# Kernel optimization log

Measured on AMD Instinct MI355X. Metric: run time of the kernel, lower is better.

Reference implementation:

```python
import jax, jax.numpy as jnp
import numpy as np

B, N, C = 8, 1024, 768
H = 12
D = C // H            # 64
HID = int(C * 4.0)    # 3072
SCALE = D ** -0.5
EPS_LN = 1e-5
EPS_BN = 1e-5


def _layernorm(x, g, b):
    mu = jnp.mean(x, axis=-1, keepdims=True)
    var = jnp.mean(jnp.square(x - mu), axis=-1, keepdims=True)
    return (x - mu) * jax.lax.rsqrt(var + EPS_LN) * g + b


def setup_inputs() -> dict:
    key = jax.random.key(0)
    ks = jax.random.split(key, 12)
    s = lambda fan: 1.0 / np.sqrt(fan)
    inp = {
        "inputs": jax.random.normal(ks[0], (B, N, C), jnp.float32),
        "ln1_g": jnp.ones((C,), jnp.float32),
        "ln1_b": jnp.zeros((C,), jnp.float32),
        # nn.Linear(dim, 3*dim, bias=False)
        "qkv_w": jax.random.uniform(ks[1], (3 * C, C), jnp.float32, -s(C), s(C)),
        # nn.Conv2d(H, H, 1, 1) head-mixing matrix
        "conv_w": jax.random.uniform(ks[2], (H, H), jnp.float32, -s(H), s(H)),
        "conv_b": jax.random.uniform(ks[3], (H,), jnp.float32, -s(H), s(H)),
        # BatchNorm2d(H) in eval mode: affine params + running stats
        "bn_g": jnp.ones((H,), jnp.float32),
        "bn_b": jnp.zeros((H,), jnp.float32),
        "bn_rm": jnp.zeros((H,), jnp.float32),
        "bn_rv": jnp.ones((H,), jnp.float32),
        "proj_w": jax.random.uniform(ks[4], (C, C), jnp.float32, -s(C), s(C)),
        "proj_b": jax.random.uniform(ks[5], (C,), jnp.float32, -s(C), s(C)),
        "ln2_g": jnp.ones((C,), jnp.float32),
        "ln2_b": jnp.zeros((C,), jnp.float32),
        "fc1_w": jax.random.uniform(ks[6], (HID, C), jnp.float32, -s(C), s(C)),
        "fc1_b": jax.random.uniform(ks[7], (HID,), jnp.float32, -s(C), s(C)),
        "fc2_w": jax.random.uniform(ks[8], (C, HID), jnp.float32, -s(HID), s(HID)),
        "fc2_b": jax.random.uniform(ks[9], (C,), jnp.float32, -s(HID), s(HID)),
    }
    return inp


def reference(inputs, ln1_g, ln1_b, qkv_w, conv_w, conv_b, bn_g, bn_b, bn_rm, bn_rv,
              proj_w, proj_b, ln2_g, ln2_b, fc1_w, fc1_b, fc2_w, fc2_b):
    # adjust_ratio = 1.0, dropouts are identity (inference), BN uses running stats (eval)
    x_ln = _layernorm(inputs, ln1_g, ln1_b)
    qkv = (x_ln @ qkv_w.T).reshape(B, N, 3, H, D).transpose(2, 0, 3, 1, 4)
    q, k, v = qkv[0], qkv[1], qkv[2]
    attn = jax.nn.softmax(jnp.einsum('bhnd,bhmd->bhnm', q, k) * SCALE, axis=-1)
    # 1x1 conv across heads then BatchNorm2d (eval) * reatten_scale(=1.0)
    attn = jnp.einsum('oh,bhnm->bonm', conv_w, attn) + conv_b[None, :, None, None]
    bn_scale = bn_g * jax.lax.rsqrt(bn_rv + EPS_BN)
    attn = (attn - bn_rm[None, :, None, None]) * bn_scale[None, :, None, None] \
        + bn_b[None, :, None, None]
    attn_next = attn
    out = jnp.einsum('bhnm,bhmd->bhnd', attn, v).transpose(0, 2, 1, 3).reshape(B, N, C)
    out = out @ proj_w.T + proj_b
    x = inputs + out
    h = _layernorm(x, ln2_g, ln2_b)
    h = jax.nn.gelu(h @ fc1_w.T + fc1_b, approximate=False)
    x = x + (h @ fc2_w.T + fc2_b)
    return (x, attn_next)
```

## Files before the change

### kernel.cpp

```cpp
#include <hip/hip_runtime.h>
#include <cmath>

#define B_   8
#define N_   1024
#define C_   768
#define H_   12
#define D_   64
#define HID_ 3072
#define M_   8192

using frag  = __attribute__((ext_vector_type(8))) short;
using f32x4 = __attribute__((ext_vector_type(4))) float;
using s4v   = __attribute__((ext_vector_type(4))) short;

__device__ __forceinline__ short f2bf(float x) {
    union { float f; unsigned u; } v; v.f = x;
    unsigned r = (v.u + 0x7FFFu + ((v.u >> 16) & 1u)) >> 16;
    return (short)r;
}
__device__ __forceinline__ float b2f(short s) {
    union { float f; unsigned u; } v; v.u = ((unsigned)(unsigned short)s) << 16;
    return v.f;
}
__device__ __forceinline__ float bfr(float x) { return b2f(f2bf(x)); }
__device__ __forceinline__ float gelu_exact(float x) {
    return 0.5f * x * (1.0f + erff(x * 0.70710678118654752f));
}
__device__ __forceinline__ void gload16(const void* g, void* l) {
    __builtin_amdgcn_global_load_lds(
        (const __attribute__((address_space(1))) void*)g,
        (__attribute__((address_space(3))) void*)l, 16, 0, 0);
}

__global__ __launch_bounds__(256)
void cvt_bf16(const float* __restrict__ src, short* __restrict__ dst, int n)
{
    int i = (blockIdx.x * 256 + threadIdx.x) * 4;
    if (i < n) {
        float4 u = *(const float4*)(src + i);
        s4v s; s[0] = f2bf(u.x); s[1] = f2bf(u.y); s[2] = f2bf(u.z); s[3] = f2bf(u.w);
        *(s4v*)(dst + i) = s;
    }
}

__global__ __launch_bounds__(256)
void ln_bf16(const float* __restrict__ x, const float* __restrict__ g,
             const float* __restrict__ b, short* __restrict__ y)
{
    __shared__ float red[256];
    const long row = blockIdx.x;
    const float* xr = x + row * C_;
    short* yr = y + row * C_;
    const int t = threadIdx.x;
    float v0 = xr[t], v1 = xr[t + 256], v2 = xr[t + 512];
    red[t] = v0 + v1 + v2;
    __syncthreads();
    for (int o = 128; o > 0; o >>= 1) { if (t < o) red[t] += red[t + o]; __syncthreads(); }
    const float mu = red[0] * (1.0f / 768.0f);
    __syncthreads();
    const float d0 = v0 - mu, d1 = v1 - mu, d2 = v2 - mu;
    red[t] = d0 * d0 + d1 * d1 + d2 * d2;
    __syncthreads();
    for (int o = 128; o > 0; o >>= 1) { if (t < o) red[t] += red[t + o]; __syncthreads(); }
    const float rstd = rsqrtf(red[0] * (1.0f / 768.0f) + 1e-5f);
    yr[t]       = f2bf(d0 * rstd * g[t]       + b[t]);
    yr[t + 256] = f2bf(d1 * rstd * g[t + 256] + b[t + 256]);
    yr[t + 512] = f2bf(d2 * rstd * g[t + 512] + b[t + 512]);
}

template<int BM, int BN, int WGM, int WGN, bool AF32, bool OUTF32, bool ACT_GELU, bool STATS>
__global__ __launch_bounds__(256)
void gemm_mfma(const void* __restrict__ Ap, int lda, long sAb, long sAh,
               const short* __restrict__ Bp, int ldb, long sBb, long sBh,
               const float* __restrict__ bias,
               const float* __restrict__ res, int ldres,
               void* __restrict__ Cp, int ldc, long sCb, long sCh,
               float2* __restrict__ st,
               int K, float alpha)
{
    constexpr int FM = BM / (WGM * 16), FN = BN / (WGN * 16);
    __shared__ short As[BM * 64];
    __shared__ short Bs[BN * 64];
    const int tid = threadIdx.x;
    const int wid = tid >> 6, lane = tid & 63;
    const int z = blockIdx.z, zb = z / H_, zh = z - zb * H_;
    const long m0 = (long)blockIdx.y * BM;
    const int  n0 = blockIdx.x * BN;
    const short* Bb = Bp + zb * sBb + zh * sBh + (long)n0 * ldb;
    const short* Abh = nullptr; const float* Afh = nullptr;
    if constexpr (AF32) Afh = (const float*)Ap + zb * sAb + zh * sAh + m0 * lda;
    else                Abh = (const short*)Ap + zb * sAb + zh * sAh + m0 * lda;
    f32x4 acc[FM][FN] = {};
    const int wr = wid / WGN, wc = wid - wr * WGN;
    const int srow = lane >> 3;
    const int schunk = (lane & 7) ^ srow;

    for (int k0 = 0; k0 < K; k0 += 64) {
        if constexpr (!AF32) {
            for (int g = wid; g < BM / 8; g += 4)
                gload16(Abh + (long)(g * 8 + srow) * lda + k0 + schunk * 8, &As[g * 512]);
        } else {
            const int r = tid >> 1, h2 = tid & 1;
            const float* sp = Afh + (long)r * lda + k0 + h2 * 32;
            #pragma unroll
            for (int j = 0; j < 4; ++j) {
                float4 u0 = *(const float4*)(sp + j * 8);
                float4 u1 = *(const float4*)(sp + j * 8 + 4);
                frag w;
                w[0] = f2bf(u0.x); w[1] = f2bf(u0.y); w[2] = f2bf(u0.z); w[3] = f2bf(u0.w);
                w[4] = f2bf(u1.x); w[5] = f2bf(u1.y); w[6] = f2bf(u1.z); w[7] = f2bf(u1.w);
                *(frag*)&As[r * 64 + (((h2 * 4 + j)) ^ (r & 7)) * 8] = w;
            }
        }
        for (int g = wid; g < BN / 8; g += 4)
            gload16(Bb + (long)(g * 8 + srow) * ldb + k0 + schunk * 8, &Bs[g * 512]);
        __syncthreads();
        #pragma unroll
        for (int kk = 0; kk < 2; ++kk) {
            frag a[FM], b[FN];
            #pragma unroll
            for (int fm = 0; fm < FM; ++fm) {
                const int r = wr * FM * 16 + fm * 16 + (lane & 15);
                const int ph = (kk * 4 + (lane >> 4)) ^ (r & 7);
                a[fm] = *(const frag*)&As[r * 64 + ph * 8];
            }
            #pragma unroll
            for (int fn = 0; fn < FN; ++fn) {
                const int r = wc * FN * 16 + fn * 16 + (lane & 15);
                const int ph = (kk * 4 + (lane >> 4)) ^ (r & 7);
                b[fn] = *(const frag*)&Bs[r * 64 + ph * 8];
            }
            #pragma unroll
            for (int fm = 0; fm < FM; ++fm)
                #pragma unroll
                for (int fn = 0; fn < FN; ++fn)
                    acc[fm][fn] = __builtin_amdgcn_mfma_f32_16x16x32_bf16(a[fm], b[fn], acc[fm][fn], 0, 0, 0);
        }
        __syncthreads();
    }

    float* Cf = (float*)Cp; short* Cs = (short*)Cp;
    const long cbase = zb * sCb + zh * sCh;
    #pragma unroll
    for (int fm = 0; fm < FM; ++fm) {
        #pragma unroll
        for (int fn = 0; fn < FN; ++fn) {
            const long rg = m0 + wr * FM * 16 + fm * 16 + ((lane >> 4) * 4);
            const int  cg = n0 + wc * FN * 16 + fn * 16 + (lane & 15);
            const float bv = bias ? bias[cg] : 0.0f;
            #pragma unroll
            for (int q = 0; q < 4; ++q) {
                const long row = rg + q;
                float v = acc[fm][fn][q] * alpha + bv;
                if (res) v += res[row * (long)ldres + cg];
                if constexpr (ACT_GELU) v = gelu_exact(v);
                if constexpr (OUTF32) Cf[cbase + row * ldc + cg] = v;
                else                  Cs[cbase + row * ldc + cg] = f2bf(v);
            }
        }
    }

    if constexpr (STATS) {
        float* sred = (float*)As;
        float tmax[FM][4];
        #pragma unroll
        for (int fm = 0; fm < FM; ++fm)
            #pragma unroll
            for (int q = 0; q < 4; ++q) {
                float v = bfr(acc[fm][0][q] * alpha);
                #pragma unroll
                for (int fn = 1; fn < FN; ++fn) v = fmaxf(v, bfr(acc[fm][fn][q] * alpha));
                v = fmaxf(v, __shfl_xor(v, 1));
                v = fmaxf(v, __shfl_xor(v, 2));
                v = fmaxf(v, __shfl_xor(v, 4));
                v = fmaxf(v, __shfl_xor(v, 8));
                const int r = wr * FM * 16 + fm * 16 + (lane >> 4) * 4 + q;
                if ((lane & 15) == 0) sred[wc * BM + r] = v;
            }
        __syncthreads();
        #pragma unroll
        for (int fm = 0; fm < FM; ++fm)
            #pragma unroll
            for (int q = 0; q < 4; ++q) {
                const int r = wr * FM * 16 + fm * 16 + (lane >> 4) * 4 + q;
                tmax[fm][q] = fmaxf(sred[r], sred[BM + r]);
            }
        __syncthreads();
        #pragma unroll
        for (int fm = 0; fm < FM; ++fm)
            #pragma unroll
            for (int q = 0; q < 4; ++q) {
                float e = 0.0f;
                #pragma unroll
                for (int fn = 0; fn < FN; ++fn)
                    e += __expf(bfr(acc[fm][fn][q] * alpha) - tmax[fm][q]);
                e += __shfl_xor(e, 1);
                e += __shfl_xor(e, 2);
                e += __shfl_xor(e, 4);
                e += __shfl_xor(e, 8);
                const int r = wr * FM * 16 + fm * 16 + (lane >> 4) * 4 + q;
                if ((lane & 15) == 0) sred[wc * BM + r] = e;
            }
        __syncthreads();
        if (wc == 0) {
            #pragma unroll
            for (int fm = 0; fm < FM; ++fm)
                #pragma unroll
                for (int q = 0; q < 4; ++q) {
                    const int r = wr * FM * 16 + fm * 16 + (lane >> 4) * 4 + q;
                    if ((lane & 15) == 0) {
                        float2 o; o.x = tmax[fm][q]; o.y = sred[r] + sred[BM + r];
                        st[((long)z * N_ + m0 + r) * 8 + blockIdx.x] = o;
                    }
                }
        }
    }
}

__global__ __launch_bounds__(256)
void smb2(const short* __restrict__ S, const float2* __restrict__ st,
          float* __restrict__ attn,
          const float* __restrict__ cw, const float* __restrict__ cb,
          const float* __restrict__ bg, const float* __restrict__ bb,
          const float* __restrict__ brm, const float* __restrict__ brv)
{
    __shared__ float coef[H_][H_], baseA[H_], scA[H_], smx[H_], sinv[H_];
    const int t = threadIdx.x;
    const int bn = blockIdx.x;
    const int b = bn >> 10, n = bn & 1023;
    if (t < H_) {
        const float s = bg[t] * rsqrtf(brv[t] + 1e-5f);
        scA[t] = s;
        baseA[t] = (cb[t] - brm[t]) * s + bb[t];
    }
    __syncthreads();
    if (t < H_ * H_) coef[t / H_][t % H_] = cw[t] * scA[t / H_];
    if (t < H_) {
        const float2* sp = st + ((long)(b * H_ + t) * N_ + n) * 8;
        float2 sv[8];
        #pragma unroll
        for (int i = 0; i < 8; ++i) sv[i] = sp[i];
        float gm = sv[0].x;
        #pragma unroll
        for (int i = 1; i < 8; ++i) gm = fmaxf(gm, sv[i].x);
        float gs = 0.0f;
        #pragma unroll
        for (int i = 0; i < 8; ++i) gs += sv[i].y * __expf(sv[i].x - gm);
        smx[t] = gm;
        sinv[t] = 1.0f / gs;
    }
    __syncthreads();

    const long pstr = (long)N_ * N_;
    const short* sb = S    + (long)b * H_ * pstr + (long)n * N_ + t * 4;
    float*       ab = attn + (long)b * H_ * pstr + (long)n * N_ + t * 4;
    float4 p[H_];
    #pragma unroll
    for (int h = 0; h < H_; ++h) {
        const s4v sv = *(const s4v*)(sb + (long)h * pstr);
        const float gm = smx[h], gi = sinv[h];
        float4 e;
        e.x = __expf(b2f(sv[0]) - gm) * gi;
        e.y = __expf(b2f(sv[1]) - gm) * gi;
        e.z = __expf(b2f(sv[2]) - gm) * gi;
        e.w = __expf(b2f(sv[3]) - gm) * gi;
        p[h] = e;
    }
    #pragma unroll
    for (int o = 0; o < H_; ++o) {
        const float bse = baseA[o];
        float4 a; a.x = bse; a.y = bse; a.z = bse; a.w = bse;
        #pragma unroll
        for (int h = 0; h < H_; ++h) {
            const float w = coef[o][h];
            a.x += w * p[h].x; a.y += w * p[h].y;
            a.z += w * p[h].z; a.w += w * p[h].w;
        }
        *(float4*)(ab + (long)o * pstr) = a;
    }
}

__global__ __launch_bounds__(256)
void vtrans(const short* __restrict__ qkv, short* __restrict__ vT)
{
    __shared__ short tile[64][72];
    const int bh = blockIdx.x;
    const int n0 = blockIdx.y * 64;
    const int b = bh / H_, h = bh - b * H_;
    const short* src = qkv + (long)b * N_ * (3 * C_) + 2 * C_ + h * D_;
    const int t = threadIdx.x;
    {
        const int r = t >> 2, c = (t & 3) * 16;
        const short* sp = src + (long)(n0 + r) * (3 * C_) + c;
        #pragma unroll
        for (int j = 0; j < 16; j++) tile[r][c + j] = sp[j];
    }
    __syncthreads();
    {
        const int d = t >> 2, c = (t & 3) * 16;
        short* dp = vT + (long)bh * (D_ * N_) + (long)d * N_ + n0 + c;
        #pragma unroll
        for (int j = 0; j < 16; j++) dp[j] = tile[c + j][d];
    }
}

extern "C" void kernel_launch(void* const* d_in, const int* in_sizes, int n_in,
                              void* d_out, int out_size, void* d_ws, size_t ws_size,
                              hipStream_t stream)
{
    const float* inp    = (const float*)d_in[0];
    const float* ln1_g  = (const float*)d_in[1];
    const float* ln1_b  = (const float*)d_in[2];
    const float* qkv_w  = (const float*)d_in[3];
    const float* conv_w = (const float*)d_in[4];
    const float* conv_b = (const float*)d_in[5];
    const float* bn_g   = (const float*)d_in[6];
    const float* bn_b   = (const float*)d_in[7];
    const float* bn_rm  = (const float*)d_in[8];
    const float* bn_rv  = (const float*)d_in[9];
    const float* proj_w = (const float*)d_in[10];
    const float* proj_b = (const float*)d_in[11];
    const float* ln2_g  = (const float*)d_in[12];
    const float* ln2_b  = (const float*)d_in[13];
    const float* fc1_w  = (const float*)d_in[14];
    const float* fc1_b  = (const float*)d_in[15];
    const float* fc2_w  = (const float*)d_in[16];
    const float* fc2_b  = (const float*)d_in[17];

    float* outx = (float*)d_out;
    float* attn = outx + (long)M_ * C_;

    char* w = (char*)d_ws;
    short* wqkv  = (short*)w;  w += (long)3 * C_ * C_ * 2;
    short* wproj = (short*)w;  w += (long)C_ * C_ * 2;
    short* wfc1  = (short*)w;  w += (long)HID_ * C_ * 2;
    short* wfc2  = (short*)w;  w += (long)C_ * HID_ * 2;
    short* xln   = (short*)w;  w += (long)M_ * C_ * 2;
    short* qkvb  = (short*)w;
    short* hbuf  = qkvb;       w += (long)M_ * HID_ * 2;
    short* vT    = (short*)w;  w += (long)B_ * H_ * D_ * N_ * 2;
    short* Obf   = (short*)w;  w += (long)M_ * C_ * 2;
    float* xres  = (float*)w;  w += (long)M_ * C_ * 4;
    float2* st   = (float2*)w; w += (long)B_ * H_ * N_ * 8 * 8;
    short* Sbf   = (short*)w;  w += (long)B_ * H_ * N_ * N_ * 2;

    cvt_bf16<<<(3 * C_ * C_) / 1024, 256, 0, stream>>>(qkv_w, wqkv, 3 * C_ * C_);
    cvt_bf16<<<(C_ * C_) / 1024,     256, 0, stream>>>(proj_w, wproj, C_ * C_);
    cvt_bf16<<<(HID_ * C_) / 1024,   256, 0, stream>>>(fc1_w, wfc1, HID_ * C_);
    cvt_bf16<<<(C_ * HID_) / 1024,   256, 0, stream>>>(fc2_w, wfc2, C_ * HID_);

    ln_bf16<<<M_, 256, 0, stream>>>(inp, ln1_g, ln1_b, xln);

    gemm_mfma<128, 128, 2, 2, false, false, false, false><<<dim3(18, 64, 1), 256, 0, stream>>>(
        xln, C_, 0, 0, wqkv, C_, 0, 0, nullptr, nullptr, 0,
        qkvb, 3 * C_, 0, 0, nullptr, C_, 1.0f);

    vtrans<<<dim3(B_ * H_, 16), 256, 0, stream>>>(qkvb, vT);

    gemm_mfma<128, 128, 2, 2, false, false, false, true><<<dim3(8, 8, 96), 256, 0, stream>>>(
        qkvb,      3 * C_, (long)N_ * 3 * C_, D_,
        qkvb + C_, 3 * C_, (long)N_ * 3 * C_, D_,
        nullptr, nullptr, 0,
        Sbf, N_, (long)H_ * N_ * N_, (long)N_ * N_, st, D_, 0.125f);

    smb2<<<M_, 256, 0, stream>>>(Sbf, st, attn, conv_w, conv_b, bn_g, bn_b, bn_rm, bn_rv);

    gemm_mfma<128, 64, 4, 1, true, false, false, false><<<dim3(1, 8, 96), 256, 0, stream>>>(
        attn, N_, (long)H_ * N_ * N_, (long)N_ * N_,
        vT, N_, (long)H_ * D_ * N_, (long)D_ * N_,
        nullptr, nullptr, 0,
        Obf, C_, (long)N_ * C_, D_, nullptr, N_, 1.0f);

    gemm_mfma<128, 128, 2, 2, false, true, false, false><<<dim3(6, 64, 1), 256, 0, stream>>>(
        Obf, C_, 0, 0, wproj, C_, 0, 0, proj_b, inp, C_,
        xres, C_, 0, 0, nullptr, C_, 1.0f);

    ln_bf16<<<M_, 256, 0, stream>>>(xres, ln2_g, ln2_b, xln);

    gemm_mfma<128, 128, 2, 2, false, false, true, false><<<dim3(24, 64, 1), 256, 0, stream>>>(
        xln, C_, 0, 0, wfc1, C_, 0, 0, fc1_b, nullptr, 0,
        hbuf, HID_, 0, 0, nullptr, C_, 1.0f);

    gemm_mfma<128, 128, 2, 2, false, true, false, false><<<dim3(6, 64, 1), 256, 0, stream>>>(
        hbuf, HID_, 0, 0, wfc2, HID_, 0, 0, fc2_b, xres, C_,
        outx, C_, 0, 0, nullptr, HID_, 1.0f);
}
```

Before: 649.3 us.

## Write bf16 attention copy in smb2, swizzle GEMM blocks across XCDs, merge weight casts

The softmax/conv/BN kernel now also writes a bf16 copy of the attention map into the score buffer. The attn@V GEMM can then load its A operand with direct global-to-LDS loads instead of reading fp32 attention and converting it in registers. GEMM workgroup IDs are remapped so consecutive tiles land on the same XCD for better L2 reuse, and the four weight-cast launches are merged into one. The cost is an extra 200MB-class bf16 write of the attention map, traded against halving the attn@V A-operand read bandwidth and its conversion work.

```diff
diff --git a/kernel.cpp b/kernel.cpp
--- a/kernel.cpp
+++ b/kernel.cpp
@@ -32,15 +32,36 @@
         (__attribute__((address_space(3))) void*)l, 16, 0, 0);
 }
 
-__global__ __launch_bounds__(256)
-void cvt_bf16(const float* __restrict__ src, short* __restrict__ dst, int n)
-{
-    int i = (blockIdx.x * 256 + threadIdx.x) * 4;
-    if (i < n) {
-        float4 u = *(const float4*)(src + i);
-        s4v s; s[0] = f2bf(u.x); s[1] = f2bf(u.y); s[2] = f2bf(u.z); s[3] = f2bf(u.w);
-        *(s4v*)(dst + i) = s;
-    }
+__device__ __forceinline__ int2 swz_xy() {
+    const int gx = gridDim.x;
+    const int nwg = gx * gridDim.y;
+    const int orig = blockIdx.y * gx + blockIdx.x;
+    const int q = nwg >> 3, r = nwg & 7;
+    const int xcd = orig & 7;
+    const int base = (xcd < r) ? xcd * (q + 1) : r * (q + 1) + (xcd - r) * q;
+    const int wgid = base + (orig >> 3);
+    int2 v; v.x = wgid % gx; v.y = wgid / gx;
+    return v;
+}
+
+#define NW0 (3 * C_ * C_)
+#define NW1 (C_ * C_)
+#define NW2 (HID_ * C_)
+#define NW3 (C_ * HID_)
+__global__ __launch_bounds__(256)
+void cvt_weights(const float* __restrict__ s0, const float* __restrict__ s1,
+                 const float* __restrict__ s2, const float* __restrict__ s3,
+                 short* __restrict__ dst)
+{
+    long i = ((long)blockIdx.x * 256 + threadIdx.x) * 4;
+    const float* s; long off;
+    if      (i < NW0)             { s = s0; off = i; }
+    else if (i < NW0 + NW1)       { s = s1; off = i - NW0; }
+    else if (i < NW0 + NW1 + NW2) { s = s2; off = i - NW0 - NW1; }
+    else                          { s = s3; off = i - NW0 - NW1 - NW2; }
+    float4 u = *(const float4*)(s + off);
+    s4v o; o[0] = f2bf(u.x); o[1] = f2bf(u.y); o[2] = f2bf(u.z); o[3] = f2bf(u.w);
+    *(s4v*)(dst + i) = o;
 }
 
 __global__ __launch_bounds__(256)
@@ -68,9 +89,9 @@
     yr[t + 512] = f2bf(d2 * rstd * g[t + 512] + b[t + 512]);
 }
 
-template<int BM, int BN, int WGM, int WGN, bool AF32, bool OUTF32, bool ACT_GELU, bool STATS>
-__global__ __launch_bounds__(256)
-void gemm_mfma(const void* __restrict__ Ap, int lda, long sAb, long sAh,
+template<int BM, int BN, int WGM, int WGN, bool OUTF32, bool ACT_GELU, bool STATS>
+__global__ __launch_bounds__(256)
+void gemm_mfma(const short* __restrict__ Ap, int lda, long sAb, long sAh,
                const short* __restrict__ Bp, int ldb, long sBb, long sBh,
                const float* __restrict__ bias,
                const float* __restrict__ res, int ldres,
@@ -84,34 +105,20 @@
     const int tid = threadIdx.x;
     const int wid = tid >> 6, lane = tid & 63;
     const int z = blockIdx.z, zb = z / H_, zh = z - zb * H_;
-    const long m0 = (long)blockIdx.y * BM;
-    const int  n0 = blockIdx.x * BN;
+    const int2 bxy = swz_xy();
+    const int bx = bxy.x, by = bxy.y;
+    const long m0 = (long)by * BM;
+    const int  n0 = bx * BN;
+    const short* Ab = Ap + zb * sAb + zh * sAh + m0 * lda;
     const short* Bb = Bp + zb * sBb + zh * sBh + (long)n0 * ldb;
-    const short* Abh = nullptr; const float* Afh = nullptr;
-    if constexpr (AF32) Afh = (const float*)Ap + zb * sAb + zh * sAh + m0 * lda;
-    else                Abh = (const short*)Ap + zb * sAb + zh * sAh + m0 * lda;
     f32x4 acc[FM][FN] = {};
     const int wr = wid / WGN, wc = wid - wr * WGN;
     const int srow = lane >> 3;
     const int schunk = (lane & 7) ^ srow;
 
     for (int k0 = 0; k0 < K; k0 += 64) {
-        if constexpr (!AF32) {
-            for (int g = wid; g < BM / 8; g += 4)
-                gload16(Abh + (long)(g * 8 + srow) * lda + k0 + schunk * 8, &As[g * 512]);
-        } else {
-            const int r = tid >> 1, h2 = tid & 1;
-            const float* sp = Afh + (long)r * lda + k0 + h2 * 32;
-            #pragma unroll
-            for (int j = 0; j < 4; ++j) {
-                float4 u0 = *(const float4*)(sp + j * 8);
-                float4 u1 = *(const float4*)(sp + j * 8 + 4);
-                frag w;
-                w[0] = f2bf(u0.x); w[1] = f2bf(u0.y); w[2] = f2bf(u0.z); w[3] = f2bf(u0.w);
-                w[4] = f2bf(u1.x); w[5] = f2bf(u1.y); w[6] = f2bf(u1.z); w[7] = f2bf(u1.w);
-                *(frag*)&As[r * 64 + (((h2 * 4 + j)) ^ (r & 7)) * 8] = w;
-            }
-        }
+        for (int g = wid; g < BM / 8; g += 4)
+            gload16(Ab + (long)(g * 8 + srow) * lda + k0 + schunk * 8, &As[g * 512]);
         for (int g = wid; g < BN / 8; g += 4)
             gload16(Bb + (long)(g * 8 + srow) * ldb + k0 + schunk * 8, &Bs[g * 512]);
         __syncthreads();
@@ -210,7 +217,7 @@
                     const int r = wr * FM * 16 + fm * 16 + (lane >> 4) * 4 + q;
                     if ((lane & 15) == 0) {
                         float2 o; o.x = tmax[fm][q]; o.y = sred[r] + sred[BM + r];
-                        st[((long)z * N_ + m0 + r) * 8 + blockIdx.x] = o;
+                        st[((long)z * N_ + m0 + r) * 8 + bx] = o;
                     }
                 }
         }
@@ -218,7 +225,7 @@
 }
 
 __global__ __launch_bounds__(256)
-void smb2(const short* __restrict__ S, const float2* __restrict__ st,
+void smb2(short* __restrict__ S, const float2* __restrict__ st,
           float* __restrict__ attn,
           const float* __restrict__ cw, const float* __restrict__ cb,
           const float* __restrict__ bg, const float* __restrict__ bb,
@@ -252,7 +259,7 @@
     __syncthreads();
 
     const long pstr = (long)N_ * N_;
-    const short* sb = S    + (long)b * H_ * pstr + (long)n * N_ + t * 4;
+    short*       sb = S    + (long)b * H_ * pstr + (long)n * N_ + t * 4;
     float*       ab = attn + (long)b * H_ * pstr + (long)n * N_ + t * 4;
     float4 p[H_];
     #pragma unroll
@@ -277,6 +284,8 @@
             a.z += w * p[h].z; a.w += w * p[h].w;
         }
         *(float4*)(ab + (long)o * pstr) = a;
+        s4v pb; pb[0] = f2bf(a.x); pb[1] = f2bf(a.y); pb[2] = f2bf(a.z); pb[3] = f2bf(a.w);
+        *(s4v*)(sb + (long)o * pstr) = pb;
     }
 }
 
@@ -331,10 +340,10 @@
     float* attn = outx + (long)M_ * C_;
 
     char* w = (char*)d_ws;
-    short* wqkv  = (short*)w;  w += (long)3 * C_ * C_ * 2;
-    short* wproj = (short*)w;  w += (long)C_ * C_ * 2;
-    short* wfc1  = (short*)w;  w += (long)HID_ * C_ * 2;
-    short* wfc2  = (short*)w;  w += (long)C_ * HID_ * 2;
+    short* wqkv  = (short*)w;  w += (long)NW0 * 2;
+    short* wproj = (short*)w;  w += (long)NW1 * 2;
+    short* wfc1  = (short*)w;  w += (long)NW2 * 2;
+    short* wfc2  = (short*)w;  w += (long)NW3 * 2;
     short* xln   = (short*)w;  w += (long)M_ * C_ * 2;
     short* qkvb  = (short*)w;
     short* hbuf  = qkvb;       w += (long)M_ * HID_ * 2;
@@ -344,20 +353,18 @@
     float2* st   = (float2*)w; w += (long)B_ * H_ * N_ * 8 * 8;
     short* Sbf   = (short*)w;  w += (long)B_ * H_ * N_ * N_ * 2;
 
-    cvt_bf16<<<(3 * C_ * C_) / 1024, 256, 0, stream>>>(qkv_w, wqkv, 3 * C_ * C_);
-    cvt_bf16<<<(C_ * C_) / 1024,     256, 0, stream>>>(proj_w, wproj, C_ * C_);
-    cvt_bf16<<<(HID_ * C_) / 1024,   256, 0, stream>>>(fc1_w, wfc1, HID_ * C_);
-    cvt_bf16<<<(C_ * HID_) / 1024,   256, 0, stream>>>(fc2_w, wfc2, C_ * HID_);
+    cvt_weights<<<(NW0 + NW1 + NW2 + NW3) / 1024, 256, 0, stream>>>(
+        qkv_w, proj_w, fc1_w, fc2_w, wqkv);
 
     ln_bf16<<<M_, 256, 0, stream>>>(inp, ln1_g, ln1_b, xln);
 
-    gemm_mfma<128, 128, 2, 2, false, false, false, false><<<dim3(18, 64, 1), 256, 0, stream>>>(
+    gemm_mfma<128, 128, 2, 2, false, false, false><<<dim3(18, 64, 1), 256, 0, stream>>>(
         xln, C_, 0, 0, wqkv, C_, 0, 0, nullptr, nullptr, 0,
         qkvb, 3 * C_, 0, 0, nullptr, C_, 1.0f);
 
     vtrans<<<dim3(B_ * H_, 16), 256, 0, stream>>>(qkvb, vT);
 
-    gemm_mfma<128, 128, 2, 2, false, false, false, true><<<dim3(8, 8, 96), 256, 0, stream>>>(
+    gemm_mfma<128, 128, 2, 2, false, false, true><<<dim3(8, 8, 96), 256, 0, stream>>>(
         qkvb,      3 * C_, (long)N_ * 3 * C_, D_,
         qkvb + C_, 3 * C_, (long)N_ * 3 * C_, D_,
         nullptr, nullptr, 0,
@@ -365,23 +372,23 @@
 
     smb2<<<M_, 256, 0, stream>>>(Sbf, st, attn, conv_w, conv_b, bn_g, bn_b, bn_rm, bn_rv);
 
-    gemm_mfma<128, 64, 4, 1, true, false, false, false><<<dim3(1, 8, 96), 256, 0, stream>>>(
-        attn, N_, (long)H_ * N_ * N_, (long)N_ * N_,
+    gemm_mfma<128, 64, 4, 1, false, false, false><<<dim3(1, 8, 96), 256, 0, stream>>>(
+        Sbf, N_, (long)H_ * N_ * N_, (long)N_ * N_,
         vT, N_, (long)H_ * D_ * N_, (long)D_ * N_,
         nullptr, nullptr, 0,
         Obf, C_, (long)N_ * C_, D_, nullptr, N_, 1.0f);
 
-    gemm_mfma<128, 128, 2, 2, false, true, false, false><<<dim3(6, 64, 1), 256, 0, stream>>>(
+    gemm_mfma<128, 128, 2, 2, true, false, false><<<dim3(6, 64, 1), 256, 0, stream>>>(
         Obf, C_, 0, 0, wproj, C_, 0, 0, proj_b, inp, C_,
         xres, C_, 0, 0, nullptr, C_, 1.0f);
 
     ln_bf16<<<M_, 256, 0, stream>>>(xres, ln2_g, ln2_b, xln);
 
-    gemm_mfma<128, 128, 2, 2, false, false, true, false><<<dim3(24, 64, 1), 256, 0, stream>>>(
+    gemm_mfma<128, 128, 2, 2, false, true, false><<<dim3(24, 64, 1), 256, 0, stream>>>(
         xln, C_, 0, 0, wfc1, C_, 0, 0, fc1_b, nullptr, 0,
         hbuf, HID_, 0, 0, nullptr, C_, 1.0f);
 
-    gemm_mfma<128, 128, 2, 2, false, true, false, false><<<dim3(6, 64, 1), 256, 0, stream>>>(
+    gemm_mfma<128, 128, 2, 2, true, false, false><<<dim3(6, 64, 1), 256, 0, stream>>>(
         hbuf, HID_, 0, 0, wfc2, HID_, 0, 0, fc2_b, xres, C_,
         outx, C_, 0, 0, nullptr, HID_, 1.0f);
 }
```

Result: faster. 611.6 us (-5.8%).
